# Optimization experiments

Measured on AMD Instinct MI355X. Metric: run time of the kernel, lower is better.

The kernel has to match this reference:

```python
import jax, jax.numpy as jnp
import numpy as np

NUM_HEADS = 16
ROPE_THETA = 10000.0


def _rope_cos_sin(seq_len, head_dim, dtype):
    # theta_i = theta^(-2i/d_k), i in [0, d_k/2)
    i = jnp.arange(head_dim // 2, dtype=jnp.float32)
    inv_freq = ROPE_THETA ** (-2.0 * i / head_dim)
    pos = jnp.arange(seq_len, dtype=jnp.float32)[:, None]
    ang = pos * inv_freq[None, :]                      # [S, d/2]
    return jnp.cos(ang).astype(dtype), jnp.sin(ang).astype(dtype)


def _apply_rope(t, cos, sin):
    # t: [B, H, S, d]; rotate consecutive pairs (complex multiply)
    B, H, S, d = t.shape
    tp = t.reshape(B, H, S, d // 2, 2)
    x0, x1 = tp[..., 0], tp[..., 1]
    r0 = x0 * cos - x1 * sin
    r1 = x0 * sin + x1 * cos
    return jnp.stack([r0, r1], axis=-1).reshape(B, H, S, d)


def setup_inputs() -> dict:
    key = jax.random.key(0)
    k1, k2, k3 = jax.random.split(key, 3)
    B, S, D = 4, 2048, 1024
    x = jax.random.normal(k1, (B, S, D), dtype=jnp.float32)
    padding_mask = jnp.ones((B, S), dtype=jnp.int32)
    # trunc-normal-ish init, std = sqrt(2/(in+out))
    std_qkv = np.sqrt(2.0 / (D + 3 * D))
    w_qkv = jax.random.normal(k2, (3 * D, D), dtype=jnp.float32) * std_qkv
    w_o = jax.random.normal(k3, (D, D), dtype=jnp.float32) * 0.02
    return {"x": x, "padding_mask": padding_mask, "w_qkv": w_qkv, "w_o": w_o}


def reference(x, padding_mask, w_qkv, w_o):
    B, S, D = x.shape
    H = NUM_HEADS
    hd = D // H
    scale = 1.0 / np.sqrt(hd)

    qkv = x @ w_qkv.T                                   # [B, S, 3D]
    q, k, v = jnp.split(qkv, 3, axis=-1)

    def to_heads(t):
        return t.reshape(B, S, H, hd).transpose(0, 2, 1, 3)  # [B, H, S, hd]

    q, k, v = to_heads(q), to_heads(k), to_heads(v)

    cos, sin = _rope_cos_sin(S, hd, x.dtype)            # [S, hd/2]
    q = _apply_rope(q, cos, sin)
    k = _apply_rope(k, cos, sin)

    scores = jnp.einsum("bhqd,bhkd->bhqk", q, k) * scale  # [B, H, S, S]

    causal = jnp.tril(jnp.ones((S, S), dtype=x.dtype))
    mask = causal[None, :, :] * padding_mask.astype(x.dtype)[:, None, :]  # [B, S, S]
    scores = jnp.where(mask[:, None, :, :] == 0, -jnp.inf, scores)

    weights = jax.nn.softmax(scores, axis=-1)
    out = jnp.einsum("bhqk,bhkd->bhqd", weights, v)     # [B, H, S, hd]
    out = out.transpose(0, 2, 1, 3).reshape(B, S, D)
    return out @ w_o.T
```

## Files before the change

### kernel.cpp

```cpp
#include <hip/hip_runtime.h>

typedef unsigned short u16;
typedef unsigned int u32;
typedef __bf16 bf16x8 __attribute__((ext_vector_type(8)));
typedef float f32x4 __attribute__((ext_vector_type(4)));

#define MFMA_BF16(a, b, c) __builtin_amdgcn_mfma_f32_16x16x32_bf16((a), (b), (c), 0, 0, 0)

#define QSCALE 0.18033688011112042f
#define M0SHIFT 24.0f


__device__ __forceinline__ u16 f2bf(float f) {
  u32 u = __builtin_bit_cast(u32, f);
  u += 0x7fffu + ((u >> 16) & 1u);
  return (u16)(u >> 16);
}

__device__ __forceinline__ void async_copy16(const void* g, void* l) {
  __builtin_amdgcn_global_load_lds(
      (__attribute__((address_space(1))) void*)g,
      (__attribute__((address_space(3))) void*)l, 16, 0, 0);
}


__global__ __launch_bounds__(256) void prep_kernel(
    const float* __restrict__ x_f, const float* __restrict__ wqkv_f,
    const float* __restrict__ wo_f, u16* __restrict__ xb,
    u16* __restrict__ wqkvb, u16* __restrict__ wob, float2* __restrict__ rope_t) {
  const int blk = blockIdx.x;
  if (blk < 12288) {
    const float* src;
    u16* dst;
    int base;
    float scale = 1.0f;
    if (blk < 8192)      { src = x_f;    dst = xb;    base = blk; }
    else if (blk < 11264){ src = wqkv_f; dst = wqkvb; base = blk - 8192;
                           if (base < 1024) scale = QSCALE; }
    else                 { src = wo_f;   dst = wob;   base = blk - 11264; }
    const int i = base * 1024 + threadIdx.x * 4;
    const float4 v = *(const float4*)(src + i);
    ushort4 o;
    o.x = f2bf(v.x * scale); o.y = f2bf(v.y * scale);
    o.z = f2bf(v.z * scale); o.w = f2bf(v.w * scale);
    *(ushort4*)(dst + i) = o;
  } else {
    const int idx = (blk - 12288) * 256 + threadIdx.x;
    const int s = idx >> 5, i = idx & 31;
    const float invf = __builtin_amdgcn_exp2f(-(float)i * 0.41524101186092027f);
    float rev = (float)s * invf * 0.15915494309189535f;
    rev -= floorf(rev);
    rope_t[idx] = make_float2(__builtin_amdgcn_cosf(rev), __builtin_amdgcn_sinf(rev));
  }
}


__device__ __forceinline__ void gemm_bt_tile(const u16* A, const u16* B, int K,
                                             int row0, int col0,
                                             u16* lds, f32x4 acc[4][4]) {
  const int tid = threadIdx.x;
  const int wave = tid >> 6;
  const int lane = tid & 63;
  const int fr = lane & 15;
  const int quad = lane >> 4;
  const int wm = (wave >> 1) * 64;
  const int wn = (wave & 1) * 64;
  u16* a_lds = lds;
  u16* b_lds = lds + 4096;

  f32x4 zero = {0.f, 0.f, 0.f, 0.f};
#pragma unroll
  for (int mt = 0; mt < 4; ++mt)
#pragma unroll
    for (int nt = 0; nt < 4; ++nt) acc[mt][nt] = zero;

  for (int k0 = 0; k0 < K; k0 += 32) {
    __syncthreads();
#pragma unroll
    for (int c = 0; c < 2; ++c) {
      const int ebase = wave * 1024 + c * 512;
      const int e = ebase + lane * 8;
      const int r = e >> 5;
      const int kk = e & 31;
      async_copy16(A + (size_t)(row0 + r) * K + k0 + kk, a_lds + ebase);
      async_copy16(B + (size_t)(col0 + r) * K + k0 + kk, b_lds + ebase);
    }
    __syncthreads();

    bf16x8 a_frag[4], b_frag[4];
#pragma unroll
    for (int t = 0; t < 4; ++t) {
      a_frag[t] = *(const bf16x8*)(a_lds + (wm + t * 16 + fr) * 32 + quad * 8);
      b_frag[t] = *(const bf16x8*)(b_lds + (wn + t * 16 + fr) * 32 + quad * 8);
    }
#pragma unroll
    for (int mt = 0; mt < 4; ++mt)
#pragma unroll
      for (int nt = 0; nt < 4; ++nt)
        acc[mt][nt] = MFMA_BF16(a_frag[mt], b_frag[nt], acc[mt][nt]);
  }
}


__global__ __launch_bounds__(256) void qkv_rope_kernel(
    const u16* __restrict__ x, const u16* __restrict__ w_qkv,
    const float2* __restrict__ rope_t,
    u16* __restrict__ q_ws, u16* __restrict__ k_ws, u16* __restrict__ vt_ws) {
  __shared__ u16 sbuf[128 * 136];
  f32x4 acc[4][4];
  const int row0 = blockIdx.y * 128;
  const int col0 = blockIdx.x * 128;
  gemm_bt_tile(x, w_qkv, 1024, row0, col0, sbuf, acc);

  const int tid = threadIdx.x;
  const int wave = tid >> 6, lane = tid & 63;
  const int fr = lane & 15, quad = lane >> 4;
  const int wm = (wave >> 1) * 64, wn = (wave & 1) * 64;
  const int region = col0 >> 10;
  const int f0 = col0 & 1023;
  const int s0r = row0 & 2047;
  const int bb = row0 >> 11;

  __syncthreads();

  if (region < 2) {
#pragma unroll
    for (int mt = 0; mt < 4; ++mt) {
#pragma unroll
      for (int nt = 0; nt < 4; ++nt) {
        const int n = wn + nt * 16 + fr;
        const int d = n & 63;
#pragma unroll
        for (int r = 0; r < 4; ++r) {
          const int m = wm + mt * 16 + quad * 4 + r;
          const float own = acc[mt][nt][r];
          const float part = __shfl_xor(own, 1);
          const int s = s0r + m;
          const float2 cssn = rope_t[s * 32 + (d >> 1)];
          const float val = (d & 1) ? (part * cssn.y + own * cssn.x)
                                    : (own * cssn.x - part * cssn.y);
          sbuf[m * 136 + n] = f2bf(val);
        }
      }
    }
    __syncthreads();
    u16* dst = (region == 0) ? q_ws : k_ws;
    const int h0 = f0 >> 6;
#pragma unroll
    for (int j = 0; j < 8; ++j) {
      const int idx2 = j * 256 + tid;
      const int hf = idx2 >> 10;
      const int m = (idx2 & 1023) >> 3;
      const int c8 = (idx2 & 7) * 8;
      const uint4 v = *(const uint4*)(sbuf + m * 136 + hf * 64 + c8);
      *(uint4*)(dst + ((size_t)(bb * 16 + h0 + hf) * 2048 + s0r + m) * 64 + c8) = v;
    }
  } else {
#pragma unroll
    for (int mt = 0; mt < 4; ++mt)
#pragma unroll
      for (int nt = 0; nt < 4; ++nt) {
        const int n = wn + nt * 16 + fr;
#pragma unroll
        for (int r = 0; r < 4; ++r) {
          const int m = wm + mt * 16 + quad * 4 + r;
          sbuf[n * 136 + m] = f2bf(acc[mt][nt][r]);
        }
      }
    __syncthreads();
    const int h0 = f0 >> 6;
#pragma unroll
    for (int j = 0; j < 8; ++j) {
      const int idx2 = j * 256 + tid;
      const int n = idx2 >> 4;
      const int mc = (idx2 & 15) * 8;
      const int h = h0 + (n >> 6);
      const int d = n & 63;
      const uint4 v = *(const uint4*)(sbuf + n * 136 + mc);
      *(uint4*)(vt_ws + ((size_t)(bb * 16 + h) * 64 + d) * 2048 + s0r + mc) = v;
    }
  }
}


__global__ __launch_bounds__(256, 4) void flash_attn_kernel(
    const u16* __restrict__ Q, const u16* __restrict__ K, const u16* __restrict__ Vt,
    const int* __restrict__ pad, u16* __restrict__ O) {
  const int S = 2048;
  const int idx = blockIdx.x;
  const int bh = idx & 63;
  const int b = bh >> 4, h = bh & 15;
  const int q0 = (15 - (idx >> 6)) * 128;
  const u16* Qh = Q + (size_t)bh * S * 64;
  const u16* Kh = K + (size_t)bh * S * 64;
  const u16* Vth = Vt + (size_t)bh * 64 * S;
  const int tid = threadIdx.x, wave = tid >> 6, lane = tid & 63;
  const int fr = lane & 15, quad = lane >> 4;

  __shared__ u16 lds_k[2 * 64 * 32];
  __shared__ u16 lds_vt[2 * 64 * 32];
  __shared__ u16 lds_p[4][32 * 76];
  __shared__ float lds_bias[64];

  const int qb = q0 + wave * 32;
  bf16x8 qfrag[2][2];
#pragma unroll
  for (int mt = 0; mt < 2; ++mt)
#pragma unroll
    for (int kk = 0; kk < 2; ++kk)
      qfrag[mt][kk] =
          *(const bf16x8*)(Qh + (size_t)(qb + mt * 16 + fr) * 64 + kk * 32 + quad * 8);

  bf16x8 ones;
#pragma unroll
  for (int j = 0; j < 8; ++j) ones[j] = (__bf16)1.0f;

  f32x4 zero = {0.f, 0.f, 0.f, 0.f};
  f32x4 o_acc[2][4], lacc[2];
#pragma unroll
  for (int mt = 0; mt < 2; ++mt) {
    lacc[mt] = zero;
#pragma unroll
    for (int nt = 0; nt < 4; ++nt) o_acc[mt][nt] = zero;
  }

  u16* pw = lds_p[wave];
  const float NEG = -__builtin_inff();

  for (int k0 = 0; k0 <= q0 + 64; k0 += 64) {
    __syncthreads();
#pragma unroll
    for (int it = 0; it < 2; ++it) {
      const int slot = it * 256 + tid;
      const int row = tid >> 2;
      const int c8 = (tid & 3) * 8;
      async_copy16(Kh + (size_t)(k0 + row) * 64 + it * 32 + c8, lds_k + slot * 8);
      async_copy16(Vth + (size_t)row * 2048 + k0 + it * 32 + c8, lds_vt + slot * 8);
    }
    if (tid < 64) lds_bias[tid] = pad[b * S + k0 + tid] ? -M0SHIFT : NEG;
    __syncthreads();

    if (k0 <= qb + 31) {
      const bool needMask = (k0 + 63 > qb);
#pragma unroll
      for (int nt = 0; nt < 4; ++nt) {
        f32x4 s0 = zero, s1 = zero;
#pragma unroll
        for (int kk = 0; kk < 2; ++kk) {
          bf16x8 bfrag =
              *(const bf16x8*)(lds_k + (kk * 64 + nt * 16 + fr) * 32 + quad * 8);
          s0 = MFMA_BF16(qfrag[0][kk], bfrag, s0);
          s1 = MFMA_BF16(qfrag[1][kk], bfrag, s1);
        }
        const float bias = lds_bias[nt * 16 + fr];
        const int col = k0 + nt * 16 + fr;
#pragma unroll
        for (int r = 0; r < 4; ++r) {
          float v0 = s0[r] + bias;
          float v1 = s1[r] + bias;
          if (needMask) {
            if (col > qb + quad * 4 + r) v0 = NEG;
            if (col > qb + 16 + quad * 4 + r) v1 = NEG;
          }
          const float p0 = __builtin_amdgcn_exp2f(v0);
          const float p1 = __builtin_amdgcn_exp2f(v1);
          pw[(quad * 4 + r) * 76 + nt * 16 + fr] =
              (u16)(__builtin_bit_cast(u32, p0) >> 16);
          pw[(16 + quad * 4 + r) * 76 + nt * 16 + fr] =
              (u16)(__builtin_bit_cast(u32, p1) >> 16);
        }
      }
      asm volatile("s_waitcnt lgkmcnt(0)" ::: "memory");

#pragma unroll
      for (int kk = 0; kk < 2; ++kk) {
        bf16x8 p0 = *(const bf16x8*)(pw + fr * 76 + kk * 32 + quad * 8);
        bf16x8 p1 = *(const bf16x8*)(pw + (16 + fr) * 76 + kk * 32 + quad * 8);
        lacc[0] = MFMA_BF16(p0, ones, lacc[0]);
        lacc[1] = MFMA_BF16(p1, ones, lacc[1]);
#pragma unroll
        for (int nt = 0; nt < 4; ++nt) {
          bf16x8 vf =
              *(const bf16x8*)(lds_vt + (kk * 64 + nt * 16 + fr) * 32 + quad * 8);
          o_acc[0][nt] = MFMA_BF16(p0, vf, o_acc[0][nt]);
          o_acc[1][nt] = MFMA_BF16(p1, vf, o_acc[1][nt]);
        }
      }
    }
  }

#pragma unroll
  for (int mt = 0; mt < 2; ++mt)
#pragma unroll
    for (int r = 0; r < 4; ++r) {
      const int row = qb + mt * 16 + quad * 4 + r;
      const float l = lacc[mt][r];
      const float rl = (l > 0.f) ? (1.0f / l) : 0.f;
#pragma unroll
      for (int nt = 0; nt < 4; ++nt)
        O[(size_t)(b * S + row) * 1024 + h * 64 + nt * 16 + fr] =
            f2bf(o_acc[mt][nt][r] * rl);
    }
}


__global__ __launch_bounds__(256) void oproj_kernel(
    const u16* __restrict__ A, const u16* __restrict__ w_o, float* __restrict__ out) {
  __shared__ u16 lds[8192];
  f32x4 acc[4][4];
  const int row0 = blockIdx.y * 128;
  const int col0 = blockIdx.x * 128;
  gemm_bt_tile(A, w_o, 1024, row0, col0, lds, acc);
  const int tid = threadIdx.x;
  const int wave = tid >> 6, lane = tid & 63;
  const int fr = lane & 15, quad = lane >> 4;
  const int wm = (wave >> 1) * 64, wn = (wave & 1) * 64;
#pragma unroll
  for (int mt = 0; mt < 4; ++mt)
#pragma unroll
    for (int nt = 0; nt < 4; ++nt) {
      const int ncol = col0 + wn + nt * 16 + fr;
#pragma unroll
      for (int r = 0; r < 4; ++r) {
        const int mrow = row0 + wm + mt * 16 + quad * 4 + r;
        out[(size_t)mrow * 1024 + ncol] = acc[mt][nt][r];
      }
    }
}


extern "C" void kernel_launch(void* const* d_in, const int* in_sizes, int n_in,
                              void* d_out, int out_size, void* d_ws, size_t ws_size,
                              hipStream_t stream) {
  const float* x_f = (const float*)d_in[0];
  const int* pad = (const int*)d_in[1];
  const float* wqkv_f = (const float*)d_in[2];
  const float* wo_f = (const float*)d_in[3];
  float* out = (float*)d_out;

  const int NX = 4 * 2048 * 1024;
  const int NWQKV = 3072 * 1024;
  const int NWO = 1024 * 1024;
  const size_t HSZ = (size_t)4 * 16 * 2048 * 64;

  u16* xb = (u16*)d_ws;
  u16* wqkvb = xb + NX;
  u16* wob = wqkvb + NWQKV;
  u16* q_ws = wob + NWO;
  u16* k_ws = q_ws + HSZ;
  u16* vt_ws = k_ws + HSZ;
  u16* attn_ws = vt_ws + HSZ;
  float2* rope_t = (float2*)(attn_ws + HSZ);

  dim3 blk(256);
  prep_kernel<<<dim3(12544), blk, 0, stream>>>(x_f, wqkv_f, wo_f, xb, wqkvb, wob, rope_t);
  qkv_rope_kernel<<<dim3(24, 64), blk, 0, stream>>>(xb, wqkvb, rope_t, q_ws, k_ws, vt_ws);
  flash_attn_kernel<<<dim3(1024), blk, 0, stream>>>(q_ws, k_ws, vt_ws, pad, attn_ws);
  oproj_kernel<<<dim3(8, 64), blk, 0, stream>>>(attn_ws, wob, out);
}
```

Baseline: 293.1 us.

## Double-buffer K/V tiles in flash attention and reorder query-tile scheduling

Adds a second LDS buffer for the K, V-transposed and padding-bias tiles, so the async global-to-LDS loads for the next key block are issued before computing the current one. This removes one of the two barriers per iteration and lets load latency overlap with MFMA work. The block-to-query-tile mapping is also changed to a serpentine order, interleaving heavy and light causal tiles across block groups for better load balance. LDS use roughly doubles for K/V, and launch bounds drop from 4 to 3 blocks per CU, which may lower occupancy.

```diff
diff --git a/kernel.cpp b/kernel.cpp
--- a/kernel.cpp
+++ b/kernel.cpp
@@ -183,24 +183,27 @@
 }
 
 
-__global__ __launch_bounds__(256, 4) void flash_attn_kernel(
+__global__ __launch_bounds__(256, 3) void flash_attn_kernel(
     const u16* __restrict__ Q, const u16* __restrict__ K, const u16* __restrict__ Vt,
     const int* __restrict__ pad, u16* __restrict__ O) {
   const int S = 2048;
   const int idx = blockIdx.x;
   const int bh = idx & 63;
   const int b = bh >> 4, h = bh & 15;
-  const int q0 = (15 - (idx >> 6)) * 128;
+  const int j = (idx >> 6) & 3;
+  const int sr = idx >> 8;
+  const int qt_rev = (sr >> 1) * 8 + ((sr & 1) ? (7 - j) : j);
+  const int q0 = (15 - qt_rev) * 128;
   const u16* Qh = Q + (size_t)bh * S * 64;
   const u16* Kh = K + (size_t)bh * S * 64;
   const u16* Vth = Vt + (size_t)bh * 64 * S;
   const int tid = threadIdx.x, wave = tid >> 6, lane = tid & 63;
   const int fr = lane & 15, quad = lane >> 4;
 
-  __shared__ u16 lds_k[2 * 64 * 32];
-  __shared__ u16 lds_vt[2 * 64 * 32];
+  __shared__ u16 lds_k[2][2 * 64 * 32];
+  __shared__ u16 lds_vt[2][2 * 64 * 32];
   __shared__ u16 lds_p[4][32 * 76];
-  __shared__ float lds_bias[64];
+  __shared__ float lds_bias[2][64];
 
   const int qb = q0 + wave * 32;
   bf16x8 qfrag[2][2];
@@ -213,7 +216,7 @@
 
   bf16x8 ones;
 #pragma unroll
-  for (int j = 0; j < 8; ++j) ones[j] = (__bf16)1.0f;
+  for (int jj = 0; jj < 8; ++jj) ones[jj] = (__bf16)1.0f;
 
   f32x4 zero = {0.f, 0.f, 0.f, 0.f};
   f32x4 o_acc[2][4], lacc[2];
@@ -227,20 +230,32 @@
   u16* pw = lds_p[wave];
   const float NEG = -__builtin_inff();
 
-  for (int k0 = 0; k0 <= q0 + 64; k0 += 64) {
-    __syncthreads();
+  auto stage = [&](int k0, int bufi) {
 #pragma unroll
     for (int it = 0; it < 2; ++it) {
       const int slot = it * 256 + tid;
       const int row = tid >> 2;
       const int c8 = (tid & 3) * 8;
-      async_copy16(Kh + (size_t)(k0 + row) * 64 + it * 32 + c8, lds_k + slot * 8);
-      async_copy16(Vth + (size_t)row * 2048 + k0 + it * 32 + c8, lds_vt + slot * 8);
-    }
-    if (tid < 64) lds_bias[tid] = pad[b * S + k0 + tid] ? -M0SHIFT : NEG;
-    __syncthreads();
+      async_copy16(Kh + (size_t)(k0 + row) * 64 + it * 32 + c8,
+                   &lds_k[bufi][slot * 8]);
+      async_copy16(Vth + (size_t)row * 2048 + k0 + it * 32 + c8,
+                   &lds_vt[bufi][slot * 8]);
+    }
+    if (tid < 64) lds_bias[bufi][tid] = pad[b * S + k0 + tid] ? -M0SHIFT : NEG;
+  };
+
+  const int kend = q0 + 64;
+  stage(0, 0);
+  __syncthreads();
+  int cur = 0;
+
+  for (int k0 = 0; k0 <= kend; k0 += 64) {
+    if (k0 < kend) stage(k0 + 64, cur ^ 1);
 
     if (k0 <= qb + 31) {
+      const u16* lk = lds_k[cur];
+      const u16* lvt = lds_vt[cur];
+      const float* lb = lds_bias[cur];
       const bool needMask = (k0 + 63 > qb);
 #pragma unroll
       for (int nt = 0; nt < 4; ++nt) {
@@ -248,11 +263,11 @@
 #pragma unroll
         for (int kk = 0; kk < 2; ++kk) {
           bf16x8 bfrag =
-              *(const bf16x8*)(lds_k + (kk * 64 + nt * 16 + fr) * 32 + quad * 8);
+              *(const bf16x8*)(lk + (kk * 64 + nt * 16 + fr) * 32 + quad * 8);
           s0 = MFMA_BF16(qfrag[0][kk], bfrag, s0);
           s1 = MFMA_BF16(qfrag[1][kk], bfrag, s1);
         }
-        const float bias = lds_bias[nt * 16 + fr];
+        const float bias = lb[nt * 16 + fr];
         const int col = k0 + nt * 16 + fr;
 #pragma unroll
         for (int r = 0; r < 4; ++r) {
@@ -281,12 +296,15 @@
 #pragma unroll
         for (int nt = 0; nt < 4; ++nt) {
           bf16x8 vf =
-              *(const bf16x8*)(lds_vt + (kk * 64 + nt * 16 + fr) * 32 + quad * 8);
+              *(const bf16x8*)(lvt + (kk * 64 + nt * 16 + fr) * 32 + quad * 8);
           o_acc[0][nt] = MFMA_BF16(p0, vf, o_acc[0][nt]);
           o_acc[1][nt] = MFMA_BF16(p1, vf, o_acc[1][nt]);
         }
       }
     }
+
+    __syncthreads();
+    cur ^= 1;
   }
 
 #pragma unroll
```

After: 289.2 us. Within noise of the previous version (-1.3%).
